# Kernel optimization log

Measured on AMD Instinct MI355X. Metric: run time of the kernel, lower is better.

The kernel has to match this reference:

```python
import jax, jax.numpy as jnp
import numpy as np

EPS = 1e-5
NUM_HEADS = 8

def layernorm(x, g, b):
    m = x.mean(-1, keepdims=True)
    v = ((x - m) ** 2).mean(-1, keepdims=True)
    return (x - m) / jnp.sqrt(v + EPS) * g + b

def mha(x, qkv_w, qkv_b, proj_w, proj_b):
    # x: [B, N, C]; weights stored [in, out] (transposed torch Linear)
    B, N, C = x.shape
    hd = C // NUM_HEADS
    scale = hd ** -0.5
    qkv = (x @ qkv_w + qkv_b).reshape(B, N, 3, NUM_HEADS, hd)
    qkv = jnp.transpose(qkv, (2, 0, 3, 1, 4))  # [3, B, H, N, hd]
    q, k, v = qkv[0], qkv[1], qkv[2]
    attn = jax.nn.softmax(jnp.einsum('bhnd,bhmd->bhnm', q, k) * scale, axis=-1)
    o = jnp.einsum('bhnm,bhmd->bhnd', attn, v)
    o = jnp.transpose(o, (0, 2, 1, 3)).reshape(B, N, C)
    return o @ proj_w + proj_b

def gelu(x):
    return jax.nn.gelu(x, approximate=False)

def setup_inputs() -> dict:
    key = jax.random.key(0)
    C, H = 512, 2048
    B, P, NI = 2, 196, 16
    N = 1 + NI * P
    ks = jax.random.split(key, 16)
    s = 0.02
    d = {
        'x': jax.random.normal(ks[0], (B, N, C), jnp.float32),
        'num_patches_per_image': P,
        'ln1_g': jnp.ones((C,)), 'ln1_b': jnp.zeros((C,)),
        'ln2_g': jnp.ones((C,)), 'ln2_b': jnp.zeros((C,)),
        'ln3_g': jnp.ones((C,)), 'ln3_b': jnp.zeros((C,)),
        'g_qkv_w': jax.random.normal(ks[1], (C, 3 * C)) * s,
        'g_qkv_b': jnp.zeros((3 * C,)),
        'g_proj_w': jax.random.normal(ks[2], (C, C)) * s,
        'g_proj_b': jnp.zeros((C,)),
        'l_qkv_w': jax.random.normal(ks[3], (C, 3 * C)) * s,
        'l_qkv_b': jnp.zeros((3 * C,)),
        'l_proj_w': jax.random.normal(ks[4], (C, C)) * s,
        'l_proj_b': jnp.zeros((C,)),
        'mlp_w1': jax.random.normal(ks[5], (C, H)) * s,
        'mlp_b1': jnp.zeros((H,)),
        'mlp_w2': jax.random.normal(ks[6], (H, C)) * s,
        'mlp_b2': jnp.zeros((C,)),
    }
    return d

def reference(x, num_patches_per_image, ln1_g, ln1_b, ln2_g, ln2_b, ln3_g, ln3_b,
              g_qkv_w, g_qkv_b, g_proj_w, g_proj_b,
              l_qkv_w, l_qkv_b, l_proj_w, l_proj_b,
              mlp_w1, mlp_b1, mlp_w2, mlp_b2):
    B, N, C = x.shape
    P = int(num_patches_per_image)
    NI = (N - 1) // P
    # global attention over all tokens (incl. CLS)
    x = x + mha(layernorm(x, ln1_g, ln1_b), g_qkv_w, g_qkv_b, g_proj_w, g_proj_b)
    cls_tok = x[:, 0:1, :]
    patches = x[:, 1:, :]
    # local attention: block-diagonal per-image mask == independent attention
    # within each image block (masked entries underflow to exactly 0 in softmax)
    pn = layernorm(patches, ln2_g, ln2_b).reshape(B * NI, P, C)
    local = mha(pn, l_qkv_w, l_qkv_b, l_proj_w, l_proj_b).reshape(B, NI * P, C)
    patches = patches + local
    x = jnp.concatenate([cls_tok, patches], axis=1)
    h = layernorm(x, ln3_g, ln3_b)
    h = gelu(h @ mlp_w1 + mlp_b1) @ mlp_w2 + mlp_b2
    return x + h
```

## Files before the change

kernel.cpp:

```cpp
#include <hip/hip_runtime.h>
#include <math.h>

typedef __attribute__((ext_vector_type(8))) short bf16x8;
typedef __attribute__((ext_vector_type(4))) short bf16x4_t;
typedef __attribute__((ext_vector_type(4))) float f32x4;
typedef __attribute__((ext_vector_type(4))) unsigned int u32x4;

typedef const __attribute__((address_space(1))) unsigned int glb_u32;
typedef __attribute__((address_space(3))) unsigned int lds_u32;
#define GLOAD_LDS16(g, l) __builtin_amdgcn_global_load_lds( \
    (glb_u32*)(const void*)(g), (lds_u32*)(void*)(l), 16, 0, 0)

static __device__ __forceinline__ float4 ld4(const float* p) {
    return *reinterpret_cast<const float4*>(p);
}
static __device__ __forceinline__ unsigned short f2bf(float f) {
    unsigned int u = __float_as_uint(f);
    u += 0x7fffu + ((u >> 16) & 1u);
    return (unsigned short)(u >> 16);
}

__global__ __launch_bounds__(64) void ln_kernel(
    const float* __restrict__ in, const float* __restrict__ g,
    const float* __restrict__ bta, unsigned short* __restrict__ out, int mode)
{
    int r = blockIdx.x;
    int lane = threadIdx.x;
    int in_r = mode ? (r + 1 + r / 3136) : r;
    const float* xp = in + (size_t)in_r * 512 + lane * 8;
    float4 v0 = ld4(xp), v1 = ld4(xp + 4);
    float s  = v0.x + v0.y + v0.z + v0.w + v1.x + v1.y + v1.z + v1.w;
    float sq = v0.x*v0.x + v0.y*v0.y + v0.z*v0.z + v0.w*v0.w
             + v1.x*v1.x + v1.y*v1.y + v1.z*v1.z + v1.w*v1.w;
    #pragma unroll
    for (int off = 32; off; off >>= 1) {
        s  += __shfl_xor(s, off);
        sq += __shfl_xor(sq, off);
    }
    float mean = s * (1.f / 512.f);
    float var  = fmaxf(sq * (1.f / 512.f) - mean * mean, 0.f);
    float rstd = rsqrtf(var + 1e-5f);
    float4 g0 = ld4(g + lane * 8),   g1 = ld4(g + lane * 8 + 4);
    float4 b0 = ld4(bta + lane * 8), b1 = ld4(bta + lane * 8 + 4);
    float o0 = (v0.x - mean) * rstd * g0.x + b0.x;
    float o1 = (v0.y - mean) * rstd * g0.y + b0.y;
    float o2 = (v0.z - mean) * rstd * g0.z + b0.z;
    float o3 = (v0.w - mean) * rstd * g0.w + b0.w;
    float o4 = (v1.x - mean) * rstd * g1.x + b1.x;
    float o5 = (v1.y - mean) * rstd * g1.y + b1.y;
    float o6 = (v1.z - mean) * rstd * g1.z + b1.z;
    float o7 = (v1.w - mean) * rstd * g1.w + b1.w;
    u32x4 pk;
    pk[0] = (unsigned int)f2bf(o0) | ((unsigned int)f2bf(o1) << 16);
    pk[1] = (unsigned int)f2bf(o2) | ((unsigned int)f2bf(o3) << 16);
    pk[2] = (unsigned int)f2bf(o4) | ((unsigned int)f2bf(o5) << 16);
    pk[3] = (unsigned int)f2bf(o6) | ((unsigned int)f2bf(o7) << 16);
    *(u32x4*)(out + (size_t)r * 512 + lane * 8) = pk;
}

struct TransArgs {
    const float* src[6];
    unsigned short* dst[6];
    int N[6], K[6], off[6];
};

__global__ __launch_bounds__(256) void transpose_all(TransArgs a)
{
    __shared__ unsigned short tile[32][34];
    int t = blockIdx.x;
    int i = 0;
    #pragma unroll
    for (int j = 1; j < 6; ++j) if (t >= a.off[j]) i = j;
    int rel = t - a.off[i];
    int tx_n = a.N[i] >> 5;
    int bx = (rel % tx_n) * 32, by = (rel / tx_n) * 32;
    const float* W = a.src[i];
    unsigned short* WT = a.dst[i];
    int K = a.K[i], N = a.N[i];
    int tx = threadIdx.x & 31, ty = threadIdx.x >> 5;
    #pragma unroll
    for (int r = 0; r < 32; r += 8)
        tile[ty + r][tx] = f2bf(W[(size_t)(by + ty + r) * N + bx + tx]);
    __syncthreads();
    #pragma unroll
    for (int r = 0; r < 32; r += 8)
        WT[(size_t)(bx + ty + r) * K + by + tx] = tile[tx][ty + r];
}

template<int BM, int BN, int OUT_BF16>
__global__ __launch_bounds__(256) void mfma_gemm(
    const unsigned short* __restrict__ A, const unsigned short* __restrict__ WT,
    const float* __restrict__ bias, const float* __restrict__ resid,
    void* __restrict__ outp, int M, int N, int K,
    int rowmap, int act,
    unsigned short* __restrict__ vt_out,
    int vtNs, unsigned int vtMagic, int vtNsP, int vtColBase)
{
    constexpr int FI = BM / 32, FJ = BN / 32;
    constexpr int AL = BM / 64, BL = BN / 64;
    __shared__ __align__(16) unsigned short As[2][BM * 32];
    __shared__ __align__(16) unsigned short Bs[2][BN * 32];

    int tid = threadIdx.x;
    int m0 = blockIdx.x * BM, n0 = blockIdx.y * BN;
    int w = tid >> 6, l = tid & 63;
    int wm = (w >> 1) * (BM / 2), wn = (w & 1) * (BN / 2);
    int lr = l & 15, lg = l >> 4;

    int lrow = l >> 2;
    int lcol = (l & 3) * 8;

    f32x4 zero = {0.f, 0.f, 0.f, 0.f};
    f32x4 acc[FI][FJ];
    #pragma unroll
    for (int i = 0; i < FI; ++i)
        #pragma unroll
        for (int j = 0; j < FJ; ++j) acc[i][j] = zero;

#define STAGE(buf, kk) do { \
    _Pragma("unroll") \
    for (int q = 0; q < AL; ++q) { \
        int rb = (w * AL + q) * 16; \
        GLOAD_LDS16(A + (size_t)(m0 + rb + lrow) * K + (kk) + lcol, \
                    &As[buf][rb * 32]); \
    } \
    _Pragma("unroll") \
    for (int q = 0; q < BL; ++q) { \
        int rb = (w * BL + q) * 16; \
        GLOAD_LDS16(WT + (size_t)(n0 + rb + lrow) * K + (kk) + lcol, \
                    &Bs[buf][rb * 32]); \
    } \
} while (0)

    int nk = K >> 5;
    STAGE(0, 0);
    STAGE(1, 32);
    for (int s = 0; s < nk; ++s) {
        int cur = s & 1;
        if (s + 1 < nk) {
            if constexpr (AL + BL == 2)
                asm volatile("s_waitcnt vmcnt(2)" ::: "memory");
            else if constexpr (AL + BL == 3)
                asm volatile("s_waitcnt vmcnt(3)" ::: "memory");
            else
                asm volatile("s_waitcnt vmcnt(4)" ::: "memory");
        } else {
            asm volatile("s_waitcnt vmcnt(0)" ::: "memory");
        }
        __builtin_amdgcn_s_barrier();

        bf16x8 af[FI], bfr[FJ];
        #pragma unroll
        for (int i = 0; i < FI; ++i)
            af[i] = *(const bf16x8*)&As[cur][(wm + i * 16 + lr) * 32 + lg * 8];
        #pragma unroll
        for (int j = 0; j < FJ; ++j)
            bfr[j] = *(const bf16x8*)&Bs[cur][(wn + j * 16 + lr) * 32 + lg * 8];
        asm volatile("s_waitcnt lgkmcnt(0)" ::: "memory");
        __builtin_amdgcn_sched_barrier(0);
        __builtin_amdgcn_s_barrier();
        if (s + 2 < nk) STAGE(cur, (s + 2) * 32);

        #pragma unroll
        for (int i = 0; i < FI; ++i)
            #pragma unroll
            for (int j = 0; j < FJ; ++j)
                acc[i][j] = __builtin_amdgcn_mfma_f32_16x16x32_bf16(
                    af[i], bfr[j], acc[i][j], 0, 0, 0);
    }
#undef STAGE

    int rowW = vt_out ? vtColBase : N;
    #pragma unroll
    for (int i = 0; i < FI; ++i) {
        #pragma unroll
        for (int r = 0; r < 4; ++r) {
            int row = m0 + wm + i * 16 + lg * 4 + r;
            if (row >= M) continue;
            int orow = rowmap ? (row + 1 + row / 3136) : row;
            #pragma unroll
            for (int j = 0; j < FJ; ++j) {
                int col = n0 + wn + j * 16 + lr;
                if (col >= N) continue;
                float v = acc[i][j][r] + bias[col];
                if (act) v = 0.5f * v * (1.f + erff(v * 0.70710678118654752f));
                if (resid) v += resid[(size_t)orow * N + col];
                if (vt_out && col >= vtColBase) {
                    unsigned int bb = (unsigned int)(((unsigned long long)(unsigned int)row * vtMagic) >> 32);
                    int nn = row - (int)bb * vtNs;
                    vt_out[((size_t)bb * 512 + (col - vtColBase)) * vtNsP + nn] = f2bf(v);
                } else if (OUT_BF16) {
                    ((unsigned short*)outp)[(size_t)orow * rowW + col] = f2bf(v);
                } else {
                    ((float*)outp)[(size_t)orow * rowW + col] = v;
                }
            }
        }
    }
}

__global__ __launch_bounds__(512) void attn_mfma8(
    const unsigned short* __restrict__ qk, const unsigned short* __restrict__ vT,
    unsigned short* __restrict__ o, int Ns, int NsP)
{
    __shared__ __align__(16) unsigned short lds[4 * 4096];

    int tid = threadIdx.x;
    int h = blockIdx.y, b = blockIdx.z;
    int mb = b * Ns;
    int l = tid & 63, w = tid >> 6;
    int qg = w & 3, kp = w >> 2;
    int g = l >> 4, c16 = l & 15;

    int qrow = blockIdx.x * 64 + qg * 16 + c16;
    int qr = (qrow < Ns ? qrow : Ns - 1) + mb;
    const unsigned short* qp = qk + (size_t)qr * 1024 + h * 64;
    bf16x8 bQ0 = *(const bf16x8*)(qp + g * 8);
    bf16x8 bQ1 = *(const bf16x8*)(qp + 32 + g * 8);

    f32x4 zero = {0.f, 0.f, 0.f, 0.f};
    f32x4 Oacc[4] = {zero, zero, zero, zero};
    float mrun = -1e30f, lrun = 0.f;

    int r0 = tid >> 3, ch = tid & 7;
    int kd = r0 * 64 + ((ch ^ ((r0 & 7) ^ (r0 >> 3))) * 8);
    const unsigned short* kbase = qk + (size_t)mb * 1024 + 512 + h * 64 + ch * 8;
    const unsigned short* vbase = vT + ((size_t)b * 512 + h * 64 + r0) * NsP + ch * 8;

    unsigned short* Kp = lds + kp * 4096;
    unsigned short* Vp = lds + 8192 + kp * 4096;

    int ka[4][2];
    #pragma unroll
    for (int f = 0; f < 4; ++f) {
        int key = 16 * f + c16;
        int swz = (key & 7) ^ (key >> 3);
        ka[f][0] = key * 64 + ((g ^ swz) * 8);
        ka[f][1] = key * 64 + (((4 + g) ^ swz) * 8);
    }
    int va[4][4];
    #pragma unroll
    for (int j = 0; j < 4; ++j) {
        int d = 16 * j + c16;
        int sd = (d & 7) ^ (d >> 3);
        #pragma unroll
        for (int t = 0; t < 4; ++t) {
            int hc = 4 * t + g;
            va[j][t] = d * 64 + (((hc >> 1) ^ sd) * 8) + ((g & 1) * 4);
        }
    }

    const float SCL = 0.125f * 1.4426950408889634f;
    int nt = (Ns + 127) >> 7;

    u32x4 kv0, kv1, vv0, vv1;
#define LOADT(kt) do { \
    int kr0 = (kt) * 128 + r0;      if (kr0 >= Ns) kr0 = Ns - 1; \
    int kr1 = (kt) * 128 + 64 + r0; if (kr1 >= Ns) kr1 = Ns - 1; \
    kv0 = *(const u32x4*)(kbase + (size_t)kr0 * 1024); \
    kv1 = *(const u32x4*)(kbase + (size_t)kr1 * 1024); \
    vv0 = *(const u32x4*)(vbase + (kt) * 128); \
    vv1 = *(const u32x4*)(vbase + (kt) * 128 + 64); \
} while (0)
#define STORET() do { \
    *(u32x4*)&lds[kd] = kv0; \
    *(u32x4*)&lds[4096 + kd] = kv1; \
    *(u32x4*)&lds[8192 + kd] = vv0; \
    *(u32x4*)&lds[12288 + kd] = vv1; \
} while (0)

    LOADT(0);
    for (int kt = 0; kt < nt; ++kt) {
        __syncthreads();
        STORET();
        __syncthreads();
        if (kt + 1 < nt) LOADT(kt + 1);

        f32x4 st[4];
        #pragma unroll
        for (int f = 0; f < 4; ++f) {
            bf16x8 a0 = *(const bf16x8*)&Kp[ka[f][0]];
            bf16x8 a1 = *(const bf16x8*)&Kp[ka[f][1]];
            f32x4 a = zero;
            a = __builtin_amdgcn_mfma_f32_16x16x32_bf16(a0, bQ0, a, 0, 0, 0);
            a = __builtin_amdgcn_mfma_f32_16x16x32_bf16(a1, bQ1, a, 0, 0, 0);
            st[f] = a;
        }

        float sv[16];
        #pragma unroll
        for (int f = 0; f < 4; ++f)
            #pragma unroll
            for (int r = 0; r < 4; ++r) sv[4 * f + r] = st[f][r];
        int valid = Ns - kt * 128 - kp * 64;
        if (valid < 64) {
            #pragma unroll
            for (int f = 0; f < 4; ++f)
                #pragma unroll
                for (int r = 0; r < 4; ++r)
                    if (16 * f + 4 * g + r >= valid) sv[4 * f + r] = -1e30f;
        }
        float m01 = fmaxf(sv[0], sv[1]), m23 = fmaxf(sv[2], sv[3]);
        float m45 = fmaxf(sv[4], sv[5]), m67 = fmaxf(sv[6], sv[7]);
        float m89 = fmaxf(sv[8], sv[9]), mab = fmaxf(sv[10], sv[11]);
        float mcd = fmaxf(sv[12], sv[13]), mef = fmaxf(sv[14], sv[15]);
        float mloc = fmaxf(fmaxf(fmaxf(m01, m23), fmaxf(m45, m67)),
                           fmaxf(fmaxf(m89, mab), fmaxf(mcd, mef)));
        if (!__all(mloc - mrun <= 64.f)) {
            mloc = fmaxf(mloc, __shfl_xor(mloc, 16));
            mloc = fmaxf(mloc, __shfl_xor(mloc, 32));
            float mnew = fmaxf(mrun, mloc);
            float sc = exp2f((mrun - mnew) * SCL);
            lrun *= sc;
            #pragma unroll
            for (int j = 0; j < 4; ++j) {
                Oacc[j][0] *= sc; Oacc[j][1] *= sc;
                Oacc[j][2] *= sc; Oacc[j][3] *= sc;
            }
            mrun = mnew;
        }
        float nl = mrun * SCL;
        #pragma unroll
        for (int e = 0; e < 16; ++e) {
            sv[e] = exp2f(fmaf(sv[e], SCL, -nl));
            lrun += sv[e];
        }

        union { unsigned int u[4]; bf16x8 v; } plo, phi;
        #pragma unroll
        for (int wi = 0; wi < 4; ++wi) {
            asm("v_cvt_pk_bf16_f32 %0, %1, %2"
                : "=v"(plo.u[wi]) : "v"(sv[2 * wi]), "v"(sv[2 * wi + 1]));
            asm("v_cvt_pk_bf16_f32 %0, %1, %2"
                : "=v"(phi.u[wi]) : "v"(sv[8 + 2 * wi]), "v"(sv[8 + 2 * wi + 1]));
        }

        #pragma unroll
        for (int j = 0; j < 4; ++j) {
            bf16x4_t t0 = *(const bf16x4_t*)&Vp[va[j][0]];
            bf16x4_t t1 = *(const bf16x4_t*)&Vp[va[j][1]];
            bf16x4_t t2 = *(const bf16x4_t*)&Vp[va[j][2]];
            bf16x4_t t3 = *(const bf16x4_t*)&Vp[va[j][3]];
            bf16x8 aVlo = __builtin_shufflevector(t0, t1, 0, 1, 2, 3, 4, 5, 6, 7);
            bf16x8 aVhi = __builtin_shufflevector(t2, t3, 0, 1, 2, 3, 4, 5, 6, 7);
            Oacc[j] = __builtin_amdgcn_mfma_f32_16x16x32_bf16(aVlo, plo.v, Oacc[j], 0, 0, 0);
            Oacc[j] = __builtin_amdgcn_mfma_f32_16x16x32_bf16(aVhi, phi.v, Oacc[j], 0, 0, 0);
        }
    }
#undef LOADT
#undef STORET

    __syncthreads();
    float* xch = (float*)&lds[0];
    float* slot = xch + (size_t)(qg * 64 + l) * 20;
    if (kp == 1) {
        #pragma unroll
        for (int j = 0; j < 4; ++j)
            *(f32x4*)(slot + 4 * j) = Oacc[j];
        slot[16] = mrun;
        slot[17] = lrun;
    }
    __syncthreads();
    if (kp == 0) {
        float m1 = slot[16], l1 = slot[17];
        float mm = fmaxf(mrun, m1);
        float s0 = exp2f((mrun - mm) * SCL);
        float s1 = exp2f((m1 - mm) * SCL);
        lrun = lrun * s0 + l1 * s1;
        #pragma unroll
        for (int j = 0; j < 4; ++j) {
            f32x4 o1 = *(const f32x4*)(slot + 4 * j);
            Oacc[j][0] = Oacc[j][0] * s0 + o1[0] * s1;
            Oacc[j][1] = Oacc[j][1] * s0 + o1[1] * s1;
            Oacc[j][2] = Oacc[j][2] * s0 + o1[2] * s1;
            Oacc[j][3] = Oacc[j][3] * s0 + o1[3] * s1;
        }
        lrun += __shfl_xor(lrun, 16);
        lrun += __shfl_xor(lrun, 32);
        if (qrow < Ns) {
            float inv = 1.f / lrun;
            unsigned short* op = o + (size_t)(mb + qrow) * 512 + h * 64;
            #pragma unroll
            for (int j = 0; j < 4; ++j) {
                unsigned int u0, u1;
                asm("v_cvt_pk_bf16_f32 %0, %1, %2"
                    : "=v"(u0) : "v"(Oacc[j][0] * inv), "v"(Oacc[j][1] * inv));
                asm("v_cvt_pk_bf16_f32 %0, %1, %2"
                    : "=v"(u1) : "v"(Oacc[j][2] * inv), "v"(Oacc[j][3] * inv));
                uint2 stv; stv.x = u0; stv.y = u1;
                *(uint2*)(op + 16 * j + 4 * g) = stv;
            }
        }
    }
}

extern "C" void kernel_launch(void* const* d_in, const int* in_sizes, int n_in,
                              void* d_out, int out_size, void* d_ws, size_t ws_size,
                              hipStream_t stream)
{
    const float* x       = (const float*)d_in[0];
    const float* ln1_g   = (const float*)d_in[2];
    const float* ln1_b   = (const float*)d_in[3];
    const float* ln2_g   = (const float*)d_in[4];
    const float* ln2_b   = (const float*)d_in[5];
    const float* ln3_g   = (const float*)d_in[6];
    const float* ln3_b   = (const float*)d_in[7];
    const float* g_qkv_w = (const float*)d_in[8];
    const float* g_qkv_b = (const float*)d_in[9];
    const float* g_proj_w= (const float*)d_in[10];
    const float* g_proj_b= (const float*)d_in[11];
    const float* l_qkv_w = (const float*)d_in[12];
    const float* l_qkv_b = (const float*)d_in[13];
    const float* l_proj_w= (const float*)d_in[14];
    const float* l_proj_b= (const float*)d_in[15];
    const float* mlp_w1  = (const float*)d_in[16];
    const float* mlp_b1  = (const float*)d_in[17];
    const float* mlp_w2  = (const float*)d_in[18];
    const float* mlp_b2  = (const float*)d_in[19];

    float* out = (float*)d_out;

    unsigned short* buf_a = (unsigned short*)d_ws;
    unsigned short* buf_b = buf_a + (size_t)6274 * 512;
    unsigned short* vTb   = buf_b + (size_t)6274 * 2048;
    unsigned short* wbf   = vTb + (size_t)3276800 + 64;
    unsigned short* g_qkv_t  = wbf;
    unsigned short* g_proj_t = g_qkv_t + 1536 * 512;
    unsigned short* l_qkv_t  = g_proj_t + 512 * 512;
    unsigned short* l_proj_t = l_qkv_t + 1536 * 512;
    unsigned short* w1_t     = l_proj_t + 512 * 512;
    unsigned short* w2_t     = w1_t + (size_t)2048 * 512;

    unsigned int M3137 = (unsigned int)((0x100000000ULL + 3136) / 3137);
    unsigned int M196  = (unsigned int)((0x100000000ULL + 195) / 196);

    TransArgs ta;
    ta.src[0] = g_qkv_w;  ta.dst[0] = g_qkv_t;  ta.N[0] = 1536; ta.K[0] = 512;  ta.off[0] = 0;
    ta.src[1] = g_proj_w; ta.dst[1] = g_proj_t; ta.N[1] = 512;  ta.K[1] = 512;  ta.off[1] = 768;
    ta.src[2] = l_qkv_w;  ta.dst[2] = l_qkv_t;  ta.N[2] = 1536; ta.K[2] = 512;  ta.off[2] = 1024;
    ta.src[3] = l_proj_w; ta.dst[3] = l_proj_t; ta.N[3] = 512;  ta.K[3] = 512;  ta.off[3] = 1792;
    ta.src[4] = mlp_w1;   ta.dst[4] = w1_t;     ta.N[4] = 2048; ta.K[4] = 512;  ta.off[4] = 2048;
    ta.src[5] = mlp_w2;   ta.dst[5] = w2_t;     ta.N[5] = 512;  ta.K[5] = 2048; ta.off[5] = 3072;
    transpose_all<<<4096, 256, 0, stream>>>(ta);

    ln_kernel<<<6274, 64, 0, stream>>>(x, ln1_g, ln1_b, buf_a, 0);
    mfma_gemm<128,128,1><<<dim3(50, 12), 256, 0, stream>>>(
        buf_a, g_qkv_t, g_qkv_b, nullptr, buf_b, 6274, 1536, 512, 0, 0,
        vTb, 3137, M3137, 3144, 1024);
    attn_mfma8<<<dim3(50, 8, 2), 512, 0, stream>>>(buf_b, vTb, buf_a, 3137, 3144);
    mfma_gemm<64,64,0><<<dim3(99, 8), 256, 0, stream>>>(
        buf_a, g_proj_t, g_proj_b, x, out, 6274, 512, 512, 0, 0,
        nullptr, 0, 0u, 0, 0);
    ln_kernel<<<6272, 64, 0, stream>>>(out, ln2_g, ln2_b, buf_a, 1);
    mfma_gemm<128,128,1><<<dim3(49, 12), 256, 0, stream>>>(
        buf_a, l_qkv_t, l_qkv_b, nullptr, buf_b, 6272, 1536, 512, 0, 0,
        vTb, 196, M196, 200, 1024);
    attn_mfma8<<<dim3(4, 8, 32), 512, 0, stream>>>(buf_b, vTb, buf_a, 196, 200);
    mfma_gemm<64,64,0><<<dim3(98, 8), 256, 0, stream>>>(
        buf_a, l_proj_t, l_proj_b, out, out, 6272, 512, 512, 1, 0,
        nullptr, 0, 0u, 0, 0);
    ln_kernel<<<6274, 64, 0, stream>>>(out, ln3_g, ln3_b, buf_a, 0);
    mfma_gemm<128,128,1><<<dim3(50, 16), 256, 0, stream>>>(
        buf_a, w1_t, mlp_b1, nullptr, buf_b, 6274, 2048, 512, 0, 1,
        nullptr, 0, 0u, 0, 0);
    mfma_gemm<64,64,0><<<dim3(99, 8), 256, 0, stream>>>(
        buf_b, w2_t, mlp_b2, out, out, 6274, 512, 2048, 0, 0,
        nullptr, 0, 0u, 0, 0);
}
```

Measured before the change: 363.9 us.

## Batch layernorm rows, approximate GELU, set MFMA priorities, retile projection GEMMs

Several unrelated tweaks land together. Layernorm now handles four rows per 256-thread block instead of one row per 64-thread block, which cuts the block count. The exact erf GELU in the MLP GEMM epilogue becomes a sigmoid-style exp2/rcp approximation, and attention raises wave priority around its MFMA sections and rewrites the max reduction as a linear chain. The output-projection and MLP2 GEMMs switch from 64x64 to 128x64 tiles, which halves the grid size. The GELU approximation departs from the exact erf form the reference specifies and may hurt accuracy.

Result: slower. 372.3 us (+2.3%).

```diff
diff --git a/kernel.cpp b/kernel.cpp
--- a/kernel.cpp
+++ b/kernel.cpp
@@ -19,13 +19,19 @@
     u += 0x7fffu + ((u >> 16) & 1u);
     return (unsigned short)(u >> 16);
 }
-
-__global__ __launch_bounds__(64) void ln_kernel(
+static __device__ __forceinline__ float gelu_f(float v) {
+    float t = exp2f(v * fmaf(v * v, 0.1029430f, 2.3022172f));
+    return v - v * __builtin_amdgcn_rcpf(t + 1.f);
+}
+
+__global__ __launch_bounds__(256) void ln_kernel(
     const float* __restrict__ in, const float* __restrict__ g,
-    const float* __restrict__ bta, unsigned short* __restrict__ out, int mode)
+    const float* __restrict__ bta, unsigned short* __restrict__ out,
+    int mode, int nrows)
 {
-    int r = blockIdx.x;
-    int lane = threadIdx.x;
+    int r = blockIdx.x * 4 + (threadIdx.x >> 6);
+    if (r >= nrows) return;
+    int lane = threadIdx.x & 63;
     int in_r = mode ? (r + 1 + r / 3136) : r;
     const float* xp = in + (size_t)in_r * 512 + lane * 8;
     float4 v0 = ld4(xp), v1 = ld4(xp + 4);
@@ -183,7 +189,7 @@
                 int col = n0 + wn + j * 16 + lr;
                 if (col >= N) continue;
                 float v = acc[i][j][r] + bias[col];
-                if (act) v = 0.5f * v * (1.f + erff(v * 0.70710678118654752f));
+                if (act) v = gelu_f(v);
                 if (resid) v += resid[(size_t)orow * N + col];
                 if (vt_out && col >= vtColBase) {
                     unsigned int bb = (unsigned int)(((unsigned long long)(unsigned int)row * vtMagic) >> 32);
@@ -277,6 +283,7 @@
         if (kt + 1 < nt) LOADT(kt + 1);
 
         f32x4 st[4];
+        __builtin_amdgcn_s_setprio(1);
         #pragma unroll
         for (int f = 0; f < 4; ++f) {
             bf16x8 a0 = *(const bf16x8*)&Kp[ka[f][0]];
@@ -286,6 +293,7 @@
             a = __builtin_amdgcn_mfma_f32_16x16x32_bf16(a1, bQ1, a, 0, 0, 0);
             st[f] = a;
         }
+        __builtin_amdgcn_s_setprio(0);
 
         float sv[16];
         #pragma unroll
@@ -300,12 +308,11 @@
                 for (int r = 0; r < 4; ++r)
                     if (16 * f + 4 * g + r >= valid) sv[4 * f + r] = -1e30f;
         }
-        float m01 = fmaxf(sv[0], sv[1]), m23 = fmaxf(sv[2], sv[3]);
-        float m45 = fmaxf(sv[4], sv[5]), m67 = fmaxf(sv[6], sv[7]);
-        float m89 = fmaxf(sv[8], sv[9]), mab = fmaxf(sv[10], sv[11]);
-        float mcd = fmaxf(sv[12], sv[13]), mef = fmaxf(sv[14], sv[15]);
-        float mloc = fmaxf(fmaxf(fmaxf(m01, m23), fmaxf(m45, m67)),
-                           fmaxf(fmaxf(m89, mab), fmaxf(mcd, mef)));
+        float mloc = sv[0];
+        #pragma unroll
+        for (int e = 1; e + 1 < 16; e += 2)
+            mloc = fmaxf(fmaxf(mloc, sv[e]), sv[e + 1]);
+        mloc = fmaxf(mloc, sv[15]);
         if (!__all(mloc - mrun <= 64.f)) {
             mloc = fmaxf(mloc, __shfl_xor(mloc, 16));
             mloc = fmaxf(mloc, __shfl_xor(mloc, 32));
@@ -335,6 +342,7 @@
                 : "=v"(phi.u[wi]) : "v"(sv[8 + 2 * wi]), "v"(sv[8 + 2 * wi + 1]));
         }
 
+        __builtin_amdgcn_s_setprio(1);
         #pragma unroll
         for (int j = 0; j < 4; ++j) {
             bf16x4_t t0 = *(const bf16x4_t*)&Vp[va[j][0]];
@@ -346,6 +354,7 @@
             Oacc[j] = __builtin_amdgcn_mfma_f32_16x16x32_bf16(aVlo, plo.v, Oacc[j], 0, 0, 0);
             Oacc[j] = __builtin_amdgcn_mfma_f32_16x16x32_bf16(aVhi, phi.v, Oacc[j], 0, 0, 0);
         }
+        __builtin_amdgcn_s_setprio(0);
     }
 #undef LOADT
 #undef STORET
@@ -443,27 +452,27 @@
     ta.src[5] = mlp_w2;   ta.dst[5] = w2_t;     ta.N[5] = 512;  ta.K[5] = 2048; ta.off[5] = 3072;
     transpose_all<<<4096, 256, 0, stream>>>(ta);
 
-    ln_kernel<<<6274, 64, 0, stream>>>(x, ln1_g, ln1_b, buf_a, 0);
+    ln_kernel<<<1569, 256, 0, stream>>>(x, ln1_g, ln1_b, buf_a, 0, 6274);
     mfma_gemm<128,128,1><<<dim3(50, 12), 256, 0, stream>>>(
         buf_a, g_qkv_t, g_qkv_b, nullptr, buf_b, 6274, 1536, 512, 0, 0,
         vTb, 3137, M3137, 3144, 1024);
     attn_mfma8<<<dim3(50, 8, 2), 512, 0, stream>>>(buf_b, vTb, buf_a, 3137, 3144);
-    mfma_gemm<64,64,0><<<dim3(99, 8), 256, 0, stream>>>(
+    mfma_gemm<128,64,0><<<dim3(50, 8), 256, 0, stream>>>(
         buf_a, g_proj_t, g_proj_b, x, out, 6274, 512, 512, 0, 0,
         nullptr, 0, 0u, 0, 0);
-    ln_kernel<<<6272, 64, 0, stream>>>(out, ln2_g, ln2_b, buf_a, 1);
+    ln_kernel<<<1568, 256, 0, stream>>>(out, ln2_g, ln2_b, buf_a, 1, 6272);
     mfma_gemm<128,128,1><<<dim3(49, 12), 256, 0, stream>>>(
         buf_a, l_qkv_t, l_qkv_b, nullptr, buf_b, 6272, 1536, 512, 0, 0,
         vTb, 196, M196, 200, 1024);
     attn_mfma8<<<dim3(4, 8, 32), 512, 0, stream>>>(buf_b, vTb, buf_a, 196, 200);
-    mfma_gemm<64,64,0><<<dim3(98, 8), 256, 0, stream>>>(
+    mfma_gemm<128,64,0><<<dim3(49, 8), 256, 0, stream>>>(
         buf_a, l_proj_t, l_proj_b, out, out, 6272, 512, 512, 1, 0,
         nullptr, 0, 0u, 0, 0);
-    ln_kernel<<<6274, 64, 0, stream>>>(out, ln3_g, ln3_b, buf_a, 0);
+    ln_kernel<<<1569, 256, 0, stream>>>(out, ln3_g, ln3_b, buf_a, 0, 6274);
     mfma_gemm<128,128,1><<<dim3(50, 16), 256, 0, stream>>>(
         buf_a, w1_t, mlp_b1, nullptr, buf_b, 6274, 2048, 512, 0, 1,
         nullptr, 0, 0u, 0, 0);
-    mfma_gemm<64,64,0><<<dim3(99, 8), 256, 0, stream>>>(
+    mfma_gemm<128,64,0><<<dim3(50, 8), 256, 0, stream>>>(
         buf_b, w2_t, mlp_b2, out, out, 6274, 512, 2048, 0, 0,
         nullptr, 0, 0u, 0, 0);
 }
```
